# Optimization experiments

Measured on AMD Instinct MI355X. Metric: run time of the kernel, lower is better.

Reference implementation:

```python
import jax, jax.numpy as jnp
import numpy as np

NEG_SLOPE = 0.2  # PyG GATConv default LeakyReLU slope


def _gat_layer(x, src, dst, W, a_src, a_dst, b, n_nodes):
    # x: [N, Fin]; W: [Fin, H*C]; a_src/a_dst: [H, C]; b: [H*C]
    H, C = a_src.shape
    h = (x @ W).reshape(n_nodes, H, C)            # [N,H,C]
    e_s = jnp.einsum('nhc,hc->nh', h, a_src)      # [N,H]
    e_d = jnp.einsum('nhc,hc->nh', h, a_dst)
    e = jax.nn.leaky_relu(e_s[src] + e_d[dst], NEG_SLOPE)   # [E,H]
    # segment softmax over edges grouped by destination node
    m = jax.ops.segment_max(e, dst, num_segments=n_nodes)   # [N,H]
    ex = jnp.exp(e - m[dst])
    denom = jax.ops.segment_sum(ex, dst, num_segments=n_nodes)
    coef = ex / denom[dst]                         # [E,H]
    out = jax.ops.segment_sum(h[src] * coef[:, :, None], dst, num_segments=n_nodes)
    return out.reshape(n_nodes, H * C) + b         # concat=True


def _xavier(key, shape):
    fan_in, fan_out = shape[0], shape[-1]
    lim = float(np.sqrt(6.0 / (fan_in + fan_out)))
    return jax.random.uniform(key, shape, jnp.float32, -lim, lim)


def setup_inputs() -> dict:
    key = jax.random.key(0)
    ks = jax.random.split(key, 24)
    N, E, Fin, G = 50000, 1600000, 128, 64
    x = jax.random.normal(ks[0], (N, Fin), jnp.float32)
    edge_index = jax.random.randint(ks[1], (2, E), 0, N, jnp.int64)
    batch = jnp.sort(jax.random.randint(ks[2], (N,), 0, G, jnp.int64))
    # (Fin, H, C) per layer
    cfg = [(128, 1, 32), (32, 2, 32), (64, 2, 64), (128, 2, 32), (64, 2, 8)]
    params = {}
    i = 3
    for li, (fi, H, C) in enumerate(cfg, 1):
        params[f'W{li}'] = _xavier(ks[i], (fi, H * C)); i += 1
        params[f'as{li}'] = _xavier(ks[i], (H, C)) ; i += 1
        params[f'ad{li}'] = _xavier(ks[i], (H, C)) ; i += 1
        params[f'b{li}'] = jnp.zeros((H * C,), jnp.float32)
    params['fcW'] = _xavier(ks[20], (16, 1))
    params['fcb'] = jnp.zeros((1,), jnp.float32)
    return dict(x=x, edge_index=edge_index, batch=batch, **params)


def reference(x, edge_index, batch,
              W1, as1, ad1, b1, W2, as2, ad2, b2, W3, as3, ad3, b3,
              W4, as4, ad4, b4, W5, as5, ad5, b5, fcW, fcb):
    N = x.shape[0]
    G = 64
    # add self-loops (PyG GATConv default add_self_loops=True)
    loop = jnp.arange(N, dtype=edge_index.dtype)
    src = jnp.concatenate([edge_index[0], loop])
    dst = jnp.concatenate([edge_index[1], loop])
    h = jax.nn.relu(_gat_layer(x, src, dst, W1, as1, ad1, b1, N))
    h = jax.nn.relu(_gat_layer(h, src, dst, W2, as2, ad2, b2, N))
    h = jax.nn.relu(_gat_layer(h, src, dst, W3, as3, ad3, b3, N))
    h = jax.nn.relu(_gat_layer(h, src, dst, W4, as4, ad4, b4, N))
    h = jax.nn.relu(_gat_layer(h, src, dst, W5, as5, ad5, b5, N))
    # global mean pool over graphs (dropout is identity at inference)
    sums = jax.ops.segment_sum(h, batch, num_segments=G)          # [G,16]
    cnt = jax.ops.segment_sum(jnp.ones((N,), h.dtype), batch, num_segments=G)
    pooled = sums / jnp.maximum(cnt, 1.0)[:, None]
    return jax.nn.sigmoid(pooled @ fcW + fcb)                     # [G,1]
```

## Files before the change

### kernel.cpp

```cpp
#include <hip/hip_runtime.h>
#include <math.h>

#define TPB 256
#define NEG_SLOPE 0.2f
#define EPB 2048
#define BK 512

static inline int cdiv_l(long a, int b){ return (int)((a + b - 1) / b); }

typedef float v2f __attribute__((ext_vector_type(2)));

__device__ __forceinline__ ushort f2bf(float f){
  unsigned u = __float_as_uint(f);
  unsigned r = u + 0x7fffu + ((u >> 16) & 1u);
  return (ushort)(r >> 16);
}
__device__ __forceinline__ float bf2f(unsigned hi16){ return __uint_as_float(hi16 << 16); }
__device__ __forceinline__ unsigned pbf2(float a, float b){
  return (unsigned)f2bf(a) | ((unsigned)f2bf(b) << 16);
}

template<int Fin, int HC, int C, typename XT>
__global__ __launch_bounds__(256) void gemm2_k(const XT* __restrict__ X,
        const float* __restrict__ W, const float* __restrict__ as_,
        const float* __restrict__ ad_, float* __restrict__ es, float* __restrict__ ed,
        unsigned char* __restrict__ Hb, int N){
  constexpr int TPN = HC / 4;
  constexpr int NPB = (256 / TPN) * 4;
  constexpr int H   = HC / C;
  constexpr int RG  = C / 4;
  __shared__ float Wl[Fin * HC];
  for (int i = threadIdx.x; i < Fin * HC; i += 256) Wl[i] = W[i];
  __syncthreads();
  const int t  = threadIdx.x;
  const int cg = t % TPN;
  const int ng = t / TPN;
  const int jt = cg * 4;
  const int nb = blockIdx.x * NPB + ng * 4;
  const XT* xr[4];
#pragma unroll
  for (int m = 0; m < 4; ++m)
    xr[m] = X + (size_t)((nb + m < N) ? nb + m : 0) * Fin;

  float acc[4][4];
#pragma unroll
  for (int m = 0; m < 4; ++m)
#pragma unroll
    for (int j = 0; j < 4; ++j) acc[m][j] = 0.f;

  for (int k = 0; k < Fin; k += 4){
    float xv[4][4];
#pragma unroll
    for (int m = 0; m < 4; ++m){
      if constexpr (sizeof(XT) == 4){
        float4 v = *(const float4*)(xr[m] + k);
        xv[m][0] = v.x; xv[m][1] = v.y; xv[m][2] = v.z; xv[m][3] = v.w;
      } else {
        uint2 u = *(const uint2*)(xr[m] + k);
        xv[m][0] = bf2f(u.x & 0xffffu); xv[m][1] = bf2f(u.x >> 16);
        xv[m][2] = bf2f(u.y & 0xffffu); xv[m][3] = bf2f(u.y >> 16);
      }
    }
#pragma unroll
    for (int kk = 0; kk < 4; ++kk){
      float w0 = Wl[(k + kk) * HC + jt + 0];
      float w1 = Wl[(k + kk) * HC + jt + 1];
      float w2 = Wl[(k + kk) * HC + jt + 2];
      float w3 = Wl[(k + kk) * HC + jt + 3];
#pragma unroll
      for (int m = 0; m < 4; ++m){
        acc[m][0] = fmaf(xv[m][kk], w0, acc[m][0]);
        acc[m][1] = fmaf(xv[m][kk], w1, acc[m][1]);
        acc[m][2] = fmaf(xv[m][kk], w2, acc[m][2]);
        acc[m][3] = fmaf(xv[m][kk], w3, acc[m][3]);
      }
    }
  }

  const int head = jt / C;
  const float* asp = as_ + head * C + (jt % C);
  const float* adp = ad_ + head * C + (jt % C);
#pragma unroll
  for (int m = 0; m < 4; ++m){
    int n = nb + m;
    bool v = (n < N);
    if (v){
      int pk8 = __builtin_amdgcn_cvt_pk_fp8_f32(acc[m][0], acc[m][1], 0, false);
      pk8     = __builtin_amdgcn_cvt_pk_fp8_f32(acc[m][2], acc[m][3], pk8, true);
      *(int*)(Hb + (size_t)n * HC + jt) = pk8;
    }
    float ps = 0.f, pd = 0.f;
#pragma unroll
    for (int j = 0; j < 4; ++j){
      ps = fmaf(acc[m][j], asp[j], ps);
      pd = fmaf(acc[m][j], adp[j], pd);
    }
#pragma unroll
    for (int off = RG >> 1; off >= 1; off >>= 1){
      ps += __shfl_xor(ps, off);
      pd += __shfl_xor(pd, off);
    }
    if (v && (cg % RG) == 0){
      es[n * H + head] = ps;
      ed[n * H + head] = pd;
    }
  }
}


__global__ __launch_bounds__(256) void bucket_hist_k(const int* __restrict__ dst,
                        int* __restrict__ bcount, int E){
  __shared__ int lh[128];
  const int t = threadIdx.x;
  for (int i = t; i < 128; i += TPB) lh[i] = 0;
  __syncthreads();
  const int c0 = blockIdx.x * EPB;
  int i1 = c0 + EPB; if (i1 > E) i1 = E;
  for (int i = c0 + t; i < i1; i += TPB)
    atomicAdd(&lh[dst[i] >> 9], 1);
  __syncthreads();
  for (int i = t; i < 128; i += TPB)
    if (lh[i]) atomicAdd(&bcount[i], lh[i]);
}

__global__ void bucket_scan_k(const int* __restrict__ bcount,
                              int* __restrict__ bbase, int* __restrict__ bcur, int K){
  __shared__ int v[128];
  const int t = threadIdx.x;
  int orig = (t < K) ? bcount[t] : 0;
  v[t] = orig; __syncthreads();
  for (int off = 1; off < 128; off <<= 1){
    int y = (t >= off) ? v[t - off] : 0;
    __syncthreads();
    v[t] += y;
    __syncthreads();
  }
  int excl = v[t] - orig;
  if (t < K){ bbase[t] = excl; bcur[t] = excl; }
}

__global__ __launch_bounds__(256) void partition_k(const int* __restrict__ src,
                        const int* __restrict__ dst,
                        int* __restrict__ bcur, unsigned* __restrict__ packed, int E){
  __shared__ int lh[128];
  __shared__ int lofs[128];
  const int t = threadIdx.x;
  for (int i = t; i < 128; i += TPB) lh[i] = 0;
  __syncthreads();
  const int c0 = blockIdx.x * EPB;
  int i1 = c0 + EPB; if (i1 > E) i1 = E;
  for (int i = c0 + t; i < i1; i += TPB)
    atomicAdd(&lh[dst[i] >> 9], 1);
  __syncthreads();
  if (t < 128){
    lofs[t] = lh[t] ? atomicAdd(&bcur[t], lh[t]) : 0;
    lh[t] = 0;
  }
  __syncthreads();
  for (int i = c0 + t; i < i1; i += TPB){
    int d = dst[i], k = d >> 9;
    int r = atomicAdd(&lh[k], 1);
    packed[lofs[k] + r] = ((unsigned)src[i] << 9) | (unsigned)(d & 511);
  }
}

__global__ __launch_bounds__(256) void bucket_csr_k(const unsigned* __restrict__ packed,
                        const int* __restrict__ bbase, const int* __restrict__ bcur,
                        int* __restrict__ row_off, int* __restrict__ csr_src,
                        int N, int E, int K){
  __shared__ int hist[BK];
  __shared__ int cur[BK];
  __shared__ int scan2[256];
  const int k = blockIdx.x;
  const int t = threadIdx.x;
  const int b0 = bbase[k], b1 = bcur[k];
  const int nb = k * BK;
  int nloc = N - nb; if (nloc > BK) nloc = BK;

  for (int i = t; i < BK; i += 256) hist[i] = 0;
  __syncthreads();
  for (int i = b0 + t; i < b1; i += 256)
    atomicAdd(&hist[packed[i] & 511u], 1);
  __syncthreads();

  int a0 = hist[2 * t], a1 = hist[2 * t + 1];
  int pair = a0 + a1;
  scan2[t] = pair; __syncthreads();
  for (int off = 1; off < 256; off <<= 1){
    int y = (t >= off) ? scan2[t - off] : 0;
    __syncthreads();
    scan2[t] += y;
    __syncthreads();
  }
  int pexcl = scan2[t] - pair;
  const int base = b0 + nb;
  int i0 = 2 * t, i1n = 2 * t + 1;
  if (i0 < nloc){
    int r = base + pexcl + i0;
    row_off[nb + i0] = r;
    csr_src[r] = nb + i0;
    cur[i0] = r + 1;
  }
  if (i1n < nloc){
    int r = base + pexcl + a0 + i1n;
    row_off[nb + i1n] = r;
    csr_src[r] = nb + i1n;
    cur[i1n] = r + 1;
  }
  if (k == K - 1 && t == 0) row_off[N] = E + N;
  __syncthreads();

  for (int i = b0 + t; i < b1; i += 256){
    unsigned pk = packed[i];
    int p = atomicAdd(&cur[pk & 511u], 1);
    csr_src[p] = (int)(pk >> 9);
  }
}


template<int H, int C>
__global__ __launch_bounds__(256) void agg_k(const int* __restrict__ csr_src,
        const int* __restrict__ row_off,
        const float* __restrict__ es, const float* __restrict__ ed,
        const unsigned char* __restrict__ Hb, const float* __restrict__ b,
        ushort* __restrict__ outp, int N){
  constexpr int HC  = H * C;
  constexpr int LPE = HC / 8;
  constexpr int EPW = 64 / LPE;
  constexpr int UN  = (EPW >= 32) ? (64 / EPW) : 4;
  __shared__ uint2 stg[4][64];
  const int lane = threadIdx.x & 63;
  const int wv   = threadIdx.x >> 6;
  const int n = blockIdx.x * 4 + wv;
  if (n >= N) return;
  const int beg = row_off[n];
  const int deg = row_off[n + 1] - beg;

  const int grp  = lane / LPE;
  const int cpos = lane % LPE;
  const int c0   = cpos * 8;
  const int hd   = c0 / C;

  float edn[H];
#pragma unroll
  for (int h = 0; h < H; ++h) edn[h] = ed[n * H + h];

  float den[H];
#pragma unroll
  for (int h = 0; h < H; ++h) den[h] = 0.f;
  float acc[8] = {0.f,0.f,0.f,0.f,0.f,0.f,0.f,0.f};

  for (int base = 0; base < deg; base += 64){
    int j = base + lane;
    unsigned wbits = 0; int sidx = 0;
    if (j < deg){
      sidx = csr_src[beg + j];
      if (H == 2){
        float2 e2 = *(const float2*)(es + sidx * 2);
        float ea = e2.x + edn[0];
        ea = ea > 0.f ? ea : ea * NEG_SLOPE;
        ea = fminf(ea, 80.f);
        float ta = __expf(ea);
        float eb = e2.y + edn[1];
        eb = eb > 0.f ? eb : eb * NEG_SLOPE;
        eb = fminf(eb, 80.f);
        float tb = __expf(eb);
        den[0] += ta; den[1] += tb;
        wbits = pbf2(ta, tb);
      } else {
        float e = es[sidx] + edn[0];
        e = e > 0.f ? e : e * NEG_SLOPE;
        e = fminf(e, 80.f);
        float t0f = __expf(e);
        den[0] += t0f;
        wbits = __float_as_uint(t0f);
      }
    }
    __asm__ volatile("s_waitcnt lgkmcnt(0)" ::: "memory");
    stg[wv][lane] = make_uint2((unsigned)sidx, wbits);
    __asm__ volatile("s_waitcnt lgkmcnt(0)" ::: "memory");

    int cnt = deg - base; if (cnt > 64) cnt = 64;
    for (int i = 0; i < cnt; i += UN * EPW){
      uint2 e[UN]; float tf[UN]; uint2 v[UN];
#pragma unroll
      for (int u = 0; u < UN; ++u) e[u] = stg[wv][i + u * EPW + grp];
#pragma unroll
      for (int u = 0; u < UN; ++u){
        if (H == 2) tf[u] = bf2f(hd ? (e[u].y >> 16) : (e[u].y & 0xffffu));
        else        tf[u] = __uint_as_float(e[u].y);
      }
#pragma unroll
      for (int u = 0; u < UN; ++u)
        v[u] = *(const uint2*)(Hb + (size_t)e[u].x * HC + c0);
#pragma unroll
      for (int u = 0; u < UN; ++u){
        v2f p0 = __builtin_amdgcn_cvt_pk_f32_fp8((int)v[u].x, false);
        v2f p1 = __builtin_amdgcn_cvt_pk_f32_fp8((int)v[u].x, true);
        v2f p2 = __builtin_amdgcn_cvt_pk_f32_fp8((int)v[u].y, false);
        v2f p3 = __builtin_amdgcn_cvt_pk_f32_fp8((int)v[u].y, true);
        acc[0] = fmaf(tf[u], p0[0], acc[0]); acc[1] = fmaf(tf[u], p0[1], acc[1]);
        acc[2] = fmaf(tf[u], p1[0], acc[2]); acc[3] = fmaf(tf[u], p1[1], acc[3]);
        acc[4] = fmaf(tf[u], p2[0], acc[4]); acc[5] = fmaf(tf[u], p2[1], acc[5]);
        acc[6] = fmaf(tf[u], p3[0], acc[6]); acc[7] = fmaf(tf[u], p3[1], acc[7]);
      }
    }
  }

  float sinv[H];
#pragma unroll
  for (int h = 0; h < H; ++h){
    float v = den[h];
#pragma unroll
    for (int off = 32; off >= 1; off >>= 1) v += __shfl_xor(v, off);
    sinv[h] = 1.f / v;
  }

#pragma unroll
  for (int off = LPE; off < 64; off <<= 1){
#pragma unroll
    for (int k = 0; k < 8; ++k) acc[k] += __shfl_xor(acc[k], off);
  }

  if (grp == 0){
    float si = sinv[hd];
    float o[8];
#pragma unroll
    for (int k = 0; k < 8; ++k){
      float v = fmaf(acc[k], si, b[c0 + k]);
      o[k] = v > 0.f ? v : 0.f;
    }
    uint4 w;
    w.x = pbf2(o[0], o[1]); w.y = pbf2(o[2], o[3]);
    w.z = pbf2(o[4], o[5]); w.w = pbf2(o[6], o[7]);
    *(uint4*)(outp + (size_t)n * HC + c0) = w;
  }
}


__global__ __launch_bounds__(256) void pool_k(const ushort* __restrict__ f,
                       const int* __restrict__ batch,
                       float* __restrict__ pooled, float* __restrict__ cnt, int N){
  __shared__ float sp[64 * 16];
  __shared__ float sc[64];
  const int t = threadIdx.x;
  for (int i = t; i < 64 * 16; i += 256) sp[i] = 0.f;
  for (int i = t; i < 64; i += 256) sc[i] = 0.f;
  __syncthreads();
  const int per = (N + gridDim.x - 1) / gridDim.x;
  const int n0 = blockIdx.x * per;
  int n1 = n0 + per; if (n1 > N) n1 = N;
  const int nloc = t >> 4, c = t & 15;
  for (int n = n0 + nloc; n < n1; n += 16){
    int g = batch[n];
    atomicAdd(&sp[g * 16 + c], bf2f(f[(size_t)n * 16 + c]));
    if (c == 0) atomicAdd(&sc[g], 1.f);
  }
  __syncthreads();
  for (int i = t; i < 64 * 16; i += 256) if (sp[i] != 0.f) atomicAdd(&pooled[i], sp[i]);
  for (int i = t; i < 64; i += 256)      if (sc[i] != 0.f) atomicAdd(&cnt[i], sc[i]);
}

__global__ void final_fc_k(const float* __restrict__ pooled, const float* __restrict__ cnt,
                           const float* __restrict__ fcW, const float* __restrict__ fcb,
                           float* __restrict__ outp){
  int g = threadIdx.x;
  if (g >= 64) return;
  float c = cnt[g]; c = c > 1.f ? c : 1.f;
  float inv = 1.0f / c;
  float acc = fcb[0];
  for (int i = 0; i < 16; ++i) acc = fmaf(pooled[g * 16 + i] * inv, fcW[i], acc);
  outp[g] = 1.0f / (1.0f + expf(-acc));
}


extern "C" void kernel_launch(void* const* d_in, const int* in_sizes, int n_in,
                              void* d_out, int out_size, void* d_ws, size_t ws_size,
                              hipStream_t stream) {
  const float* x    = (const float*)d_in[0];
  const int*  ei    = (const int*)d_in[1];
  const int*  batch = (const int*)d_in[2];

  const int N = in_sizes[0] / 128;
  const int E = in_sizes[1] / 2;

  const int* src = ei;
  const int* dst = ei + E;

  const float* W_[5];  const float* as_[5]; const float* ad_[5]; const float* b_[5];
  for (int l = 0; l < 5; ++l) {
    W_[l]  = (const float*)d_in[3 + 4 * l + 0];
    as_[l] = (const float*)d_in[3 + 4 * l + 1];
    ad_[l] = (const float*)d_in[3 + 4 * l + 2];
    b_[l]  = (const float*)d_in[3 + 4 * l + 3];
  }
  const float* fcW = (const float*)d_in[23];
  const float* fcb = (const float*)d_in[24];
  float* outp = (float*)d_out;

  ushort*        f_buf  = (ushort*)d_ws;
  unsigned char* Hb     = (unsigned char*)(f_buf + (size_t)N * 128);
  float*         es     = (float*)(Hb + (size_t)N * 128);
  float*         ed     = es + (size_t)N * 2;
  float*         pooled = ed + (size_t)N * 2;
  float*         cnt    = pooled + 64 * 16;
  int*           bcount = (int*)(cnt + 64);
  int*           bbase  = bcount + 128;
  int*           bcur   = bbase + 128;
  int*           row_off= bcur + 128;
  int*           csr_src= row_off + N + 1;
  unsigned*      packed = (unsigned*)(csr_src + E + N);

  const int K    = (N + BK - 1) / BK;
  const int nch  = cdiv_l(E, EPB);

  hipMemsetAsync(bcount, 0, 128 * 4, stream);
  bucket_hist_k<<<nch, TPB, 0, stream>>>(dst, bcount, E);
  bucket_scan_k<<<1, 128, 0, stream>>>(bcount, bbase, bcur, K);
  partition_k<<<nch, TPB, 0, stream>>>(src, dst, bcur, packed, E);
  bucket_csr_k<<<K, 256, 0, stream>>>(packed, bbase, bcur, row_off, csr_src, N, E, K);

  const int gb = cdiv_l(N, 4);

  gemm2_k<128,32,32,float><<<cdiv_l(N, 4096/32), 256, 0, stream>>>(x, W_[0], as_[0], ad_[0], es, ed, Hb, N);
  agg_k<1,32><<<gb, 256, 0, stream>>>(csr_src, row_off, es, ed, Hb, b_[0], f_buf, N);
  gemm2_k<32,64,32,ushort><<<cdiv_l(N, 4096/64), 256, 0, stream>>>(f_buf, W_[1], as_[1], ad_[1], es, ed, Hb, N);
  agg_k<2,32><<<gb, 256, 0, stream>>>(csr_src, row_off, es, ed, Hb, b_[1], f_buf, N);
  gemm2_k<64,128,64,ushort><<<cdiv_l(N, 4096/128), 256, 0, stream>>>(f_buf, W_[2], as_[2], ad_[2], es, ed, Hb, N);
  agg_k<2,64><<<gb, 256, 0, stream>>>(csr_src, row_off, es, ed, Hb, b_[2], f_buf, N);
  gemm2_k<128,64,32,ushort><<<cdiv_l(N, 4096/64), 256, 0, stream>>>(f_buf, W_[3], as_[3], ad_[3], es, ed, Hb, N);
  agg_k<2,32><<<gb, 256, 0, stream>>>(csr_src, row_off, es, ed, Hb, b_[3], f_buf, N);
  gemm2_k<64,16,8,ushort><<<cdiv_l(N, 4096/16), 256, 0, stream>>>(f_buf, W_[4], as_[4], ad_[4], es, ed, Hb, N);
  agg_k<2,8><<<gb, 256, 0, stream>>>(csr_src, row_off, es, ed, Hb, b_[4], f_buf, N);

  hipMemsetAsync(pooled, 0, (64 * 16 + 64) * 4, stream);
  pool_k<<<64, 256, 0, stream>>>(f_buf, batch, pooled, cnt, N);
  final_fc_k<<<1, 64, 0, stream>>>(pooled, cnt, fcW, fcb, outp);
}
```

Measured before the change: 350.3 us.

## Replace scalar FMA node-feature GEMM with bf16 MFMA 16x16x32 kernel

Rewrites the per-layer projection GEMM to use bf16 MFMA instructions. Each wave computes 16 nodes across all output columns, with W stored transposed in LDS as bf16. The attention-logit dot products are then reduced across lane groups with shuffles. This cuts the scalar FMA cost of the projections, but the weights and the layer-1 fp32 inputs are now rounded to bf16, and the grid and block tiling change.

New measurement: 313.3 us. 1.12x faster.

```diff
diff --git a/kernel.cpp b/kernel.cpp
--- a/kernel.cpp
+++ b/kernel.cpp
@@ -9,6 +9,8 @@
 static inline int cdiv_l(long a, int b){ return (int)((a + b - 1) / b); }
 
 typedef float v2f __attribute__((ext_vector_type(2)));
+typedef short bf16x8 __attribute__((ext_vector_type(8)));
+typedef float f32x4 __attribute__((ext_vector_type(4)));
 
 __device__ __forceinline__ ushort f2bf(float f){
   unsigned u = __float_as_uint(f);
@@ -21,88 +23,84 @@
 }
 
 template<int Fin, int HC, int C, typename XT>
-__global__ __launch_bounds__(256) void gemm2_k(const XT* __restrict__ X,
+__global__ __launch_bounds__(256) void gemm3_k(const XT* __restrict__ X,
         const float* __restrict__ W, const float* __restrict__ as_,
         const float* __restrict__ ad_, float* __restrict__ es, float* __restrict__ ed,
         unsigned char* __restrict__ Hb, int N){
-  constexpr int TPN = HC / 4;
-  constexpr int NPB = (256 / TPN) * 4;
-  constexpr int H   = HC / C;
-  constexpr int RG  = C / 4;
-  __shared__ float Wl[Fin * HC];
-  for (int i = threadIdx.x; i < Fin * HC; i += 256) Wl[i] = W[i];
-  __syncthreads();
-  const int t  = threadIdx.x;
-  const int cg = t % TPN;
-  const int ng = t / TPN;
-  const int jt = cg * 4;
-  const int nb = blockIdx.x * NPB + ng * 4;
-  const XT* xr[4];
-#pragma unroll
-  for (int m = 0; m < 4; ++m)
-    xr[m] = X + (size_t)((nb + m < N) ? nb + m : 0) * Fin;
-
-  float acc[4][4];
-#pragma unroll
-  for (int m = 0; m < 4; ++m)
-#pragma unroll
-    for (int j = 0; j < 4; ++j) acc[m][j] = 0.f;
-
-  for (int k = 0; k < Fin; k += 4){
-    float xv[4][4];
-#pragma unroll
-    for (int m = 0; m < 4; ++m){
-      if constexpr (sizeof(XT) == 4){
-        float4 v = *(const float4*)(xr[m] + k);
-        xv[m][0] = v.x; xv[m][1] = v.y; xv[m][2] = v.z; xv[m][3] = v.w;
-      } else {
-        uint2 u = *(const uint2*)(xr[m] + k);
-        xv[m][0] = bf2f(u.x & 0xffffu); xv[m][1] = bf2f(u.x >> 16);
-        xv[m][2] = bf2f(u.y & 0xffffu); xv[m][3] = bf2f(u.y >> 16);
-      }
-    }
-#pragma unroll
-    for (int kk = 0; kk < 4; ++kk){
-      float w0 = Wl[(k + kk) * HC + jt + 0];
-      float w1 = Wl[(k + kk) * HC + jt + 1];
-      float w2 = Wl[(k + kk) * HC + jt + 2];
-      float w3 = Wl[(k + kk) * HC + jt + 3];
-#pragma unroll
-      for (int m = 0; m < 4; ++m){
-        acc[m][0] = fmaf(xv[m][kk], w0, acc[m][0]);
-        acc[m][1] = fmaf(xv[m][kk], w1, acc[m][1]);
-        acc[m][2] = fmaf(xv[m][kk], w2, acc[m][2]);
-        acc[m][3] = fmaf(xv[m][kk], w3, acc[m][3]);
-      }
-    }
-  }
-
-  const int head = jt / C;
-  const float* asp = as_ + head * C + (jt % C);
-  const float* adp = ad_ + head * C + (jt % C);
-#pragma unroll
-  for (int m = 0; m < 4; ++m){
-    int n = nb + m;
-    bool v = (n < N);
-    if (v){
-      int pk8 = __builtin_amdgcn_cvt_pk_fp8_f32(acc[m][0], acc[m][1], 0, false);
-      pk8     = __builtin_amdgcn_cvt_pk_fp8_f32(acc[m][2], acc[m][3], pk8, true);
-      *(int*)(Hb + (size_t)n * HC + jt) = pk8;
-    }
-    float ps = 0.f, pd = 0.f;
+  constexpr int H  = HC / C;
+  constexpr int NC = HC / 16;
+  constexpr int KS = Fin / 32;
+  __shared__ ushort Wt[HC][Fin + 4];
+  __shared__ float asl[HC], adl[HC];
+  for (int idx = threadIdx.x; idx < Fin * HC; idx += 256){
+    int k = idx / HC, c = idx - k * HC;
+    Wt[c][k] = f2bf(W[idx]);
+  }
+  for (int i = threadIdx.x; i < HC; i += 256){ asl[i] = as_[i]; adl[i] = ad_[i]; }
+  __syncthreads();
+
+  const int lane = threadIdx.x & 63;
+  const int wv   = threadIdx.x >> 6;
+  const int n0 = (blockIdx.x * 4 + wv) * 16;
+  if (n0 >= N) return;
+  const int nl = lane & 15;
+  const int kg = lane >> 4;
+  const int n  = n0 + nl;
+  const bool valid = (n < N);
+  const int nc = valid ? n : (N - 1);
+
+  f32x4 acc[NC];
+#pragma unroll
+  for (int ct = 0; ct < NC; ++ct) acc[ct] = (f32x4){0.f, 0.f, 0.f, 0.f};
+
+  for (int ks = 0; ks < KS; ++ks){
+    const int k0 = ks * 32 + kg * 8;
+    bf16x8 bfrag;
+    if constexpr (sizeof(XT) == 2){
+      bfrag = *(const bf16x8*)(X + (size_t)nc * Fin + k0);
+    } else {
+      float4 xa = *(const float4*)(X + (size_t)nc * Fin + k0);
+      float4 xb = *(const float4*)(X + (size_t)nc * Fin + k0 + 4);
+      bfrag[0] = (short)f2bf(xa.x); bfrag[1] = (short)f2bf(xa.y);
+      bfrag[2] = (short)f2bf(xa.z); bfrag[3] = (short)f2bf(xa.w);
+      bfrag[4] = (short)f2bf(xb.x); bfrag[5] = (short)f2bf(xb.y);
+      bfrag[6] = (short)f2bf(xb.z); bfrag[7] = (short)f2bf(xb.w);
+    }
+#pragma unroll
+    for (int ct = 0; ct < NC; ++ct){
+      bf16x8 afrag = *(const bf16x8*)(&Wt[ct * 16 + nl][k0]);
+      acc[ct] = __builtin_amdgcn_mfma_f32_16x16x32_bf16(afrag, bfrag, acc[ct], 0, 0, 0);
+    }
+  }
+
+  float ps[H], pd[H];
+#pragma unroll
+  for (int h = 0; h < H; ++h){ ps[h] = 0.f; pd[h] = 0.f; }
+#pragma unroll
+  for (int ct = 0; ct < NC; ++ct){
+    const int c0 = ct * 16 + kg * 4;
+    int pk8 = __builtin_amdgcn_cvt_pk_fp8_f32(acc[ct][0], acc[ct][1], 0, false);
+    pk8     = __builtin_amdgcn_cvt_pk_fp8_f32(acc[ct][2], acc[ct][3], pk8, true);
+    if (valid) *(int*)(Hb + (size_t)n * HC + c0) = pk8;
+    const int hd = c0 / C;
+    float s = 0.f, d = 0.f;
 #pragma unroll
     for (int j = 0; j < 4; ++j){
-      ps = fmaf(acc[m][j], asp[j], ps);
-      pd = fmaf(acc[m][j], adp[j], pd);
-    }
-#pragma unroll
-    for (int off = RG >> 1; off >= 1; off >>= 1){
-      ps += __shfl_xor(ps, off);
-      pd += __shfl_xor(pd, off);
-    }
-    if (v && (cg % RG) == 0){
-      es[n * H + head] = ps;
-      ed[n * H + head] = pd;
+      s = fmaf(acc[ct][j], asl[c0 + j], s);
+      d = fmaf(acc[ct][j], adl[c0 + j], d);
+    }
+    ps[hd] += s; pd[hd] += d;
+  }
+#pragma unroll
+  for (int h = 0; h < H; ++h){
+    ps[h] += __shfl_xor(ps[h], 16); ps[h] += __shfl_xor(ps[h], 32);
+    pd[h] += __shfl_xor(pd[h], 16); pd[h] += __shfl_xor(pd[h], 32);
+  }
+  if (valid && lane < 16){
+#pragma unroll
+    for (int h = 0; h < H; ++h){
+      es[n * H + h] = ps[h];
+      ed[n * H + h] = pd[h];
     }
   }
 }
@@ -421,16 +419,17 @@
   bucket_csr_k<<<K, 256, 0, stream>>>(packed, bbase, bcur, row_off, csr_src, N, E, K);
 
   const int gb = cdiv_l(N, 4);
-
-  gemm2_k<128,32,32,float><<<cdiv_l(N, 4096/32), 256, 0, stream>>>(x, W_[0], as_[0], ad_[0], es, ed, Hb, N);
+  const int gg = cdiv_l(N, 64);
+
+  gemm3_k<128,32,32,float><<<gg, 256, 0, stream>>>(x, W_[0], as_[0], ad_[0], es, ed, Hb, N);
   agg_k<1,32><<<gb, 256, 0, stream>>>(csr_src, row_off, es, ed, Hb, b_[0], f_buf, N);
-  gemm2_k<32,64,32,ushort><<<cdiv_l(N, 4096/64), 256, 0, stream>>>(f_buf, W_[1], as_[1], ad_[1], es, ed, Hb, N);
+  gemm3_k<32,64,32,ushort><<<gg, 256, 0, stream>>>(f_buf, W_[1], as_[1], ad_[1], es, ed, Hb, N);
   agg_k<2,32><<<gb, 256, 0, stream>>>(csr_src, row_off, es, ed, Hb, b_[1], f_buf, N);
-  gemm2_k<64,128,64,ushort><<<cdiv_l(N, 4096/128), 256, 0, stream>>>(f_buf, W_[2], as_[2], ad_[2], es, ed, Hb, N);
+  gemm3_k<64,128,64,ushort><<<gg, 256, 0, stream>>>(f_buf, W_[2], as_[2], ad_[2], es, ed, Hb, N);
   agg_k<2,64><<<gb, 256, 0, stream>>>(csr_src, row_off, es, ed, Hb, b_[2], f_buf, N);
-  gemm2_k<128,64,32,ushort><<<cdiv_l(N, 4096/64), 256, 0, stream>>>(f_buf, W_[3], as_[3], ad_[3], es, ed, Hb, N);
+  gemm3_k<128,64,32,ushort><<<gg, 256, 0, stream>>>(f_buf, W_[3], as_[3], ad_[3], es, ed, Hb, N);
   agg_k<2,32><<<gb, 256, 0, stream>>>(csr_src, row_off, es, ed, Hb, b_[3], f_buf, N);
-  gemm2_k<64,16,8,ushort><<<cdiv_l(N, 4096/16), 256, 0, stream>>>(f_buf, W_[4], as_[4], ad_[4], es, ed, Hb, N);
+  gemm3_k<64,16,8,ushort><<<gg, 256, 0, stream>>>(f_buf, W_[4], as_[4], ad_[4], es, ed, Hb, N);
   agg_k<2,8><<<gb, 256, 0, stream>>>(csr_src, row_off, es, ed, Hb, b_[4], f_buf, N);
 
   hipMemsetAsync(pooled, 0, (64 * 16 + 64) * 4, stream);
```
